# Optimization experiments

Measured on AMD Instinct MI355X. Metric: run time of the kernel, lower is better.

## Reference

```python
import jax, jax.numpy as jnp
import numpy as np

N, E, D_IN, H = 100000, 1000000, 128, 64


def setup_inputs() -> dict:
    key = jax.random.key(0)
    ks = jax.random.split(key, 8)
    return {
        "x": jax.random.normal(ks[0], (N, D_IN), dtype=jnp.float32),
        "edge_index": jax.random.randint(ks[1], (2, E), 0, N, dtype=jnp.int64),
        "W1": jax.random.normal(ks[2], (H, D_IN), dtype=jnp.float32) * (1.0 / np.sqrt(D_IN)),
        "b1": jax.random.normal(ks[3], (H,), dtype=jnp.float32) * 0.05,
        "Wmu": jax.random.normal(ks[4], (H, H), dtype=jnp.float32) * (1.0 / np.sqrt(H)),
        "bmu": jax.random.normal(ks[5], (H,), dtype=jnp.float32) * 0.05,
        "Wlv": jax.random.normal(ks[6], (H, H), dtype=jnp.float32) * (1.0 / np.sqrt(H)),
        "blv": jax.random.normal(ks[7], (H,), dtype=jnp.float32) * 0.05,
    }


def reference(x, edge_index, W1, b1, Wmu, bmu, Wlv, blv):
    n = x.shape[0]
    # GCNConv (PyG defaults): add self-loops, symmetric normalization
    loop = jnp.arange(n, dtype=edge_index.dtype)
    src = jnp.concatenate([edge_index[0], loop])  # [E+N]
    dst = jnp.concatenate([edge_index[1], loop])  # [E+N]
    deg = jax.ops.segment_sum(jnp.ones(src.shape[0], dtype=x.dtype), dst, num_segments=n)
    dinv = jnp.where(deg > 0, jax.lax.rsqrt(deg), 0.0)  # deg^{-1/2}
    norm = dinv[src] * dinv[dst]  # [E+N]
    h = x @ W1.T  # [N, H] linear transform before aggregation
    msg = h[src] * norm[:, None]  # gather + scale, [E+N, H]
    agg = jax.ops.segment_sum(msg, dst, num_segments=n) + b1  # scatter-add + bias
    h = jax.nn.relu(agg)
    return (h @ Wmu.T + bmu, h @ Wlv.T + blv)
```

## Files before the change

kernel.cpp:

```cpp
#include <hip/hip_runtime.h>

#define DIN 128
#define HDIM 64
#define SLAB 32
#define OVF_CAP 65536
#define EPT 4

__device__ __forceinline__ unsigned short f2bf(float f) {
    unsigned u = __float_as_uint(f);
    unsigned r = (u + 0x7fffu + ((u >> 16) & 1u)) >> 16;
    return (unsigned short)r;
}
__device__ __forceinline__ float lo16f(unsigned v) { return __uint_as_float(v << 16); }
__device__ __forceinline__ float hi16f(unsigned v) { return __uint_as_float(v & 0xffff0000u); }

__global__ __launch_bounds__(256) void k_scatter(const int* __restrict__ src,
                                                 const int* __restrict__ dst,
                                                 int* __restrict__ cursor,
                                                 int* __restrict__ slab,
                                                 int* __restrict__ ovf,
                                                 int* __restrict__ govf, int E) {
    int base = blockIdx.x * (256 * EPT) + threadIdx.x;
    int d[EPT], s[EPT], p[EPT];
    bool ok[EPT];
    #pragma unroll
    for (int q = 0; q < EPT; ++q) {
        int e = base + q * 256;
        ok[q] = e < E;
        d[q] = ok[q] ? dst[e] : 0;
        s[q] = ok[q] ? src[e] : 0;
    }
    #pragma unroll
    for (int q = 0; q < EPT; ++q)
        if (ok[q]) p[q] = atomicAdd(&cursor[d[q]], 1);
    #pragma unroll
    for (int q = 0; q < EPT; ++q) {
        if (ok[q]) {
            if (p[q] < SLAB) {
                slab[(size_t)d[q] * SLAB + p[q]] = s[q];
            } else {
                int o = atomicAdd(govf, 1);
                if (o < OVF_CAP) { ovf[2 * o] = d[q]; ovf[2 * o + 1] = s[q]; }
            }
        }
    }
}

__global__ __launch_bounds__(256) void k_h1(const float* __restrict__ x,
                                            const float* __restrict__ W1,
                                            const int* __restrict__ cursor,
                                            unsigned short* __restrict__ hs_bf, int n) {
    __shared__ float4 xs[64 * 32];
    __shared__ float4 ws[64 * 32];
    int t = threadIdx.x;
    int ty = t >> 4;
    int tx = t & 15;
    int nodeBase = blockIdx.x * 64;

    const float4* W14 = (const float4*)W1;
    #pragma unroll
    for (int i = 0; i < 8; ++i) {
        int f = t + i * 256;
        int r = f >> 5, c4 = f & 31;
        ws[r * 32 + (c4 ^ (r & 7))] = W14[f];
    }
    const float4* x4 = (const float4*)(x + (size_t)nodeBase * DIN);
    int limf4 = (n - nodeBase) * (DIN / 4);
    #pragma unroll
    for (int i = 0; i < 8; ++i) {
        int f = t + i * 256;
        int r = f >> 5, c4 = f & 31;
        float4 v = make_float4(0.f, 0.f, 0.f, 0.f);
        if (f < limf4) v = x4[f];
        xs[r * 32 + (c4 ^ (r & 7))] = v;
    }
    __syncthreads();

    float acc[4][4] = {};
    #pragma unroll 8
    for (int k4 = 0; k4 < 32; ++k4) {
        float4 xa[4], wb[4];
        #pragma unroll
        for (int i = 0; i < 4; ++i) {
            int r = ty + 16 * i;
            xa[i] = xs[r * 32 + (k4 ^ (r & 7))];
        }
        #pragma unroll
        for (int j = 0; j < 4; ++j) {
            int r = tx + 16 * j;
            wb[j] = ws[r * 32 + (k4 ^ (r & 7))];
        }
        #pragma unroll
        for (int i = 0; i < 4; ++i)
            #pragma unroll
            for (int j = 0; j < 4; ++j)
                acc[i][j] += xa[i].x * wb[j].x + xa[i].y * wb[j].y +
                             xa[i].z * wb[j].z + xa[i].w * wb[j].w;
    }

    #pragma unroll
    for (int i = 0; i < 4; ++i) {
        int node = nodeBase + ty + 16 * i;
        if (node < n) {
            float dn = rsqrtf((float)cursor[node] + 1.0f);
            #pragma unroll
            for (int j = 0; j < 4; ++j)
                hs_bf[(size_t)node * HDIM + tx + 16 * j] = f2bf(acc[i][j] * dn);
        }
    }
}

__global__ __launch_bounds__(256) void k_gather(const int* __restrict__ cursor,
                                                const int* __restrict__ slab,
                                                const unsigned short* __restrict__ hs_bf,
                                                float* __restrict__ h, int n) {
    int tid = threadIdx.x;
    int lane = tid & 63, wave = tid >> 6;
    int grp = lane >> 4;
    int w = lane & 15;
    const int NPW = 8;
    int base = blockIdx.x * (4 * NPW) + wave * NPW;
    for (int nn = 0; nn < NPW; ++nn) {
        int node = base + nn;
        if (node >= n) break;
        int c = cursor[node];
        int cs = (c < SLAB) ? c : SLAB;
        int sv = (lane < cs) ? slab[(size_t)node * SLAB + lane] : 0;
        uint2 v0 = *(const uint2*)(hs_bf + ((size_t)node << 6) + 4 * w);
        float sw = (grp == 0) ? 1.f : 0.f;
        float a0 = sw * lo16f(v0.x), a1 = sw * hi16f(v0.x);
        float a2 = sw * lo16f(v0.y), a3 = sw * hi16f(v0.y);
        int nfull = cs >> 2;
        for (int q = 0; q < nfull; ++q) {
            int s = __shfl(sv, 4 * q + grp);
            uint2 v = *(const uint2*)(hs_bf + ((size_t)s << 6) + 4 * w);
            a0 += lo16f(v.x); a1 += hi16f(v.x);
            a2 += lo16f(v.y); a3 += hi16f(v.y);
        }
        int r = cs & 3;
        if (r) {
            int e = 4 * nfull + grp;
            float wt = (grp < r) ? 1.f : 0.f;
            int s = __shfl(sv, (e < SLAB) ? e : 0);
            uint2 v = *(const uint2*)(hs_bf + ((size_t)s << 6) + 4 * w);
            a0 += wt * lo16f(v.x); a1 += wt * hi16f(v.x);
            a2 += wt * lo16f(v.y); a3 += wt * hi16f(v.y);
        }
        a0 += __shfl_xor(a0, 16); a0 += __shfl_xor(a0, 32);
        a1 += __shfl_xor(a1, 16); a1 += __shfl_xor(a1, 32);
        a2 += __shfl_xor(a2, 16); a2 += __shfl_xor(a2, 32);
        a3 += __shfl_xor(a3, 16); a3 += __shfl_xor(a3, 32);
        if (lane < 16)
            *(float4*)(h + ((size_t)node << 6) + 4 * w) = make_float4(a0, a1, a2, a3);
    }
}

__global__ __launch_bounds__(256) void k_overflow(const int* __restrict__ govf,
                                                  const int* __restrict__ ovf,
                                                  const unsigned short* __restrict__ hs_bf,
                                                  float* __restrict__ h) {
    int novf = govf[0];
    if (novf > OVF_CAP) novf = OVF_CAP;
    int wid = (blockIdx.x * 256 + threadIdx.x) >> 6;
    int lane = threadIdx.x & 63;
    int nw = (gridDim.x * 256) >> 6;
    for (int i = wid; i < novf; i += nw) {
        int d = ovf[2 * i], s = ovf[2 * i + 1];
        atomicAdd(&h[(size_t)d * HDIM + lane],
                  lo16f((unsigned)hs_bf[(size_t)s * HDIM + lane]));
    }
}

__global__ __launch_bounds__(256) void k_out(const float* __restrict__ h,
                                             const int* __restrict__ cursor,
                                             const float* __restrict__ b1,
                                             const float* __restrict__ Wmu,
                                             const float* __restrict__ bmu,
                                             const float* __restrict__ Wlv,
                                             const float* __restrict__ blv,
                                             float* __restrict__ out, int n) {
    __shared__ float4 xs[64 * 16];
    __shared__ float4 ws[128 * 16];
    int t = threadIdx.x;
    int ty = t >> 4;
    int tx = t & 15;
    int nodeBase = blockIdx.x * 64;

    const float4* Wm4 = (const float4*)Wmu;
    const float4* Wl4 = (const float4*)Wlv;
    #pragma unroll
    for (int i = 0; i < 4; ++i) {
        int f = t + i * 256;
        int r = f >> 4, c4 = f & 15;
        ws[r * 16 + (c4 ^ (r & 15))] = Wm4[f];
        int r2 = r + 64;
        ws[r2 * 16 + (c4 ^ (r2 & 15))] = Wl4[f];
    }
    const float4* h4 = (const float4*)(h + (size_t)nodeBase * HDIM);
    int limf4 = (n - nodeBase) * (HDIM / 4);
    #pragma unroll
    for (int i = 0; i < 4; ++i) {
        int f = t + i * 256;
        int r = f >> 4, c4 = f & 15;
        float4 v = make_float4(0.f, 0.f, 0.f, 0.f);
        if (f < limf4) {
            v = h4[f];
            float dn = rsqrtf((float)cursor[nodeBase + r] + 1.0f);
            float4 bb = ((const float4*)b1)[c4];
            v.x = fmaxf(fmaf(v.x, dn, bb.x), 0.f);
            v.y = fmaxf(fmaf(v.y, dn, bb.y), 0.f);
            v.z = fmaxf(fmaf(v.z, dn, bb.z), 0.f);
            v.w = fmaxf(fmaf(v.w, dn, bb.w), 0.f);
        }
        xs[r * 16 + (c4 ^ (r & 15))] = v;
    }
    float bias[8];
    #pragma unroll
    for (int j = 0; j < 8; ++j) {
        int o = tx + 16 * j;
        bias[j] = (o < 64) ? bmu[o] : blv[o - 64];
    }
    __syncthreads();

    float acc[4][8] = {};
    #pragma unroll 4
    for (int k4 = 0; k4 < 16; ++k4) {
        float4 xa[4], wb[8];
        #pragma unroll
        for (int i = 0; i < 4; ++i) {
            int r = ty + 16 * i;
            xa[i] = xs[r * 16 + (k4 ^ (r & 15))];
        }
        #pragma unroll
        for (int j = 0; j < 8; ++j) {
            int r = tx + 16 * j;
            wb[j] = ws[r * 16 + (k4 ^ (r & 15))];
        }
        #pragma unroll
        for (int i = 0; i < 4; ++i)
            #pragma unroll
            for (int j = 0; j < 8; ++j)
                acc[i][j] += xa[i].x * wb[j].x + xa[i].y * wb[j].y +
                             xa[i].z * wb[j].z + xa[i].w * wb[j].w;
    }

    #pragma unroll
    for (int i = 0; i < 4; ++i) {
        int node = nodeBase + ty + 16 * i;
        if (node < n) {
            #pragma unroll
            for (int j = 0; j < 8; ++j) {
                int o = tx + 16 * j;
                float val = acc[i][j] + bias[j];
                if (o < 64)
                    out[(size_t)node * HDIM + o] = val;
                else
                    out[(size_t)n * HDIM + (size_t)node * HDIM + (o - 64)] = val;
            }
        }
    }
}

extern "C" void kernel_launch(void* const* d_in, const int* in_sizes, int n_in,
                              void* d_out, int out_size, void* d_ws, size_t ws_size,
                              hipStream_t stream) {
    const float* x   = (const float*)d_in[0];
    const int*   ei  = (const int*)d_in[1];
    const float* W1  = (const float*)d_in[2];
    const float* b1  = (const float*)d_in[3];
    const float* Wmu = (const float*)d_in[4];
    const float* bmu = (const float*)d_in[5];
    const float* Wlv = (const float*)d_in[6];
    const float* blv = (const float*)d_in[7];
    float* out = (float*)d_out;

    const int N = in_sizes[0] / DIN;
    const int E = in_sizes[1] / 2;
    const int* src = ei;
    const int* dst = ei + E;

    auto align256 = [](size_t b) { return (b + 255) & ~(size_t)255; };
    char* ws = (char*)d_ws;
    size_t off = 0;
    int* cursor = (int*)(ws + off); off += align256((size_t)N * 4);
    int* govf   = (int*)(ws + off); off += 256;
    int* slab   = (int*)(ws + off); off += align256((size_t)N * SLAB * 4);
    int* ovf    = (int*)(ws + off); off += align256((size_t)OVF_CAP * 2 * 4);
    unsigned short* hs_bf = (unsigned short*)(ws + off);
    off += align256((size_t)N * HDIM * 2);
    float* h = (float*)(ws + off); off += align256((size_t)N * HDIM * 4);

    hipMemsetAsync(cursor, 0, align256((size_t)N * 4) + 256, stream);

    k_scatter<<<(E + 256 * EPT - 1) / (256 * EPT), 256, 0, stream>>>(src, dst, cursor,
                                                                     slab, ovf, govf, E);
    k_h1<<<(N + 63) / 64, 256, 0, stream>>>(x, W1, cursor, hs_bf, N);
    k_gather<<<(N + 31) / 32, 256, 0, stream>>>(cursor, slab, hs_bf, h, N);
    k_overflow<<<8, 256, 0, stream>>>(govf, ovf, hs_bf, h);
    k_out<<<(N + 63) / 64, 256, 0, stream>>>(h, cursor, b1, Wmu, bmu, Wlv, blv, out, N);
}
```

Measured before the change: 179.5 us.

## Merge edge scatter and x@W1 into one launch, add separate degree-scale pass

The edge-bucketing scatter and the x@W1 GEMM now run as one launch, with the block index choosing the role, so the atomic-heavy scatter and the compute-bound GEMM can overlap. The GEMM no longer depends on the degree counts, so the deg^-1/2 scaling moves into a new k_scale pass over hs_bf. That pass adds an extra read-modify-write of the bf16 buffer and a second bf16 rounding. The GEMM shared tile is halved into two K chunks, and the gather now uses 16-byte loads with 8 neighbours per wave step instead of 4.

```diff
diff --git a/kernel.cpp b/kernel.cpp
--- a/kernel.cpp
+++ b/kernel.cpp
@@ -14,100 +14,114 @@
 __device__ __forceinline__ float lo16f(unsigned v) { return __uint_as_float(v << 16); }
 __device__ __forceinline__ float hi16f(unsigned v) { return __uint_as_float(v & 0xffff0000u); }
 
-__global__ __launch_bounds__(256) void k_scatter(const int* __restrict__ src,
-                                                 const int* __restrict__ dst,
-                                                 int* __restrict__ cursor,
-                                                 int* __restrict__ slab,
-                                                 int* __restrict__ ovf,
-                                                 int* __restrict__ govf, int E) {
-    int base = blockIdx.x * (256 * EPT) + threadIdx.x;
-    int d[EPT], s[EPT], p[EPT];
-    bool ok[EPT];
-    #pragma unroll
-    for (int q = 0; q < EPT; ++q) {
-        int e = base + q * 256;
-        ok[q] = e < E;
-        d[q] = ok[q] ? dst[e] : 0;
-        s[q] = ok[q] ? src[e] : 0;
-    }
-    #pragma unroll
-    for (int q = 0; q < EPT; ++q)
-        if (ok[q]) p[q] = atomicAdd(&cursor[d[q]], 1);
-    #pragma unroll
-    for (int q = 0; q < EPT; ++q) {
-        if (ok[q]) {
-            if (p[q] < SLAB) {
-                slab[(size_t)d[q] * SLAB + p[q]] = s[q];
-            } else {
-                int o = atomicAdd(govf, 1);
-                if (o < OVF_CAP) { ovf[2 * o] = d[q]; ovf[2 * o + 1] = s[q]; }
+__global__ __launch_bounds__(256) void k_scatter_h1(
+        const int* __restrict__ src, const int* __restrict__ dst,
+        int* __restrict__ cursor, int* __restrict__ slab,
+        int* __restrict__ ovf, int* __restrict__ govf, int E,
+        const float* __restrict__ x, const float* __restrict__ W1,
+        unsigned short* __restrict__ hs_bf, int n, int scatBlocks) {
+    __shared__ float4 xs[64 * 16];
+    __shared__ float4 ws[64 * 16];
+    int t = threadIdx.x;
+
+    if ((int)blockIdx.x < scatBlocks) {
+        int base = blockIdx.x * (256 * EPT) + t;
+        int d[EPT], s[EPT], p[EPT];
+        bool ok[EPT];
+        #pragma unroll
+        for (int q = 0; q < EPT; ++q) {
+            int e = base + q * 256;
+            ok[q] = e < E;
+            d[q] = ok[q] ? dst[e] : 0;
+            s[q] = ok[q] ? src[e] : 0;
+        }
+        #pragma unroll
+        for (int q = 0; q < EPT; ++q)
+            if (ok[q]) p[q] = atomicAdd(&cursor[d[q]], 1);
+        #pragma unroll
+        for (int q = 0; q < EPT; ++q) {
+            if (ok[q]) {
+                if (p[q] < SLAB) {
+                    slab[(size_t)d[q] * SLAB + p[q]] = s[q];
+                } else {
+                    int o = atomicAdd(govf, 1);
+                    if (o < OVF_CAP) { ovf[2 * o] = d[q]; ovf[2 * o + 1] = s[q]; }
+                }
             }
         }
-    }
-}
-
-__global__ __launch_bounds__(256) void k_h1(const float* __restrict__ x,
-                                            const float* __restrict__ W1,
-                                            const int* __restrict__ cursor,
-                                            unsigned short* __restrict__ hs_bf, int n) {
-    __shared__ float4 xs[64 * 32];
-    __shared__ float4 ws[64 * 32];
-    int t = threadIdx.x;
+        return;
+    }
+
+    int bid = blockIdx.x - scatBlocks;
     int ty = t >> 4;
     int tx = t & 15;
-    int nodeBase = blockIdx.x * 64;
-
+    int nodeBase = bid * 64;
     const float4* W14 = (const float4*)W1;
-    #pragma unroll
-    for (int i = 0; i < 8; ++i) {
-        int f = t + i * 256;
-        int r = f >> 5, c4 = f & 31;
-        ws[r * 32 + (c4 ^ (r & 7))] = W14[f];
-    }
     const float4* x4 = (const float4*)(x + (size_t)nodeBase * DIN);
     int limf4 = (n - nodeBase) * (DIN / 4);
-    #pragma unroll
-    for (int i = 0; i < 8; ++i) {
-        int f = t + i * 256;
-        int r = f >> 5, c4 = f & 31;
-        float4 v = make_float4(0.f, 0.f, 0.f, 0.f);
-        if (f < limf4) v = x4[f];
-        xs[r * 32 + (c4 ^ (r & 7))] = v;
-    }
-    __syncthreads();
 
     float acc[4][4] = {};
-    #pragma unroll 8
-    for (int k4 = 0; k4 < 32; ++k4) {
-        float4 xa[4], wb[4];
+    #pragma unroll
+    for (int kc = 0; kc < 2; ++kc) {
         #pragma unroll
         for (int i = 0; i < 4; ++i) {
-            int r = ty + 16 * i;
-            xa[i] = xs[r * 32 + (k4 ^ (r & 7))];
-        }
-        #pragma unroll
-        for (int j = 0; j < 4; ++j) {
-            int r = tx + 16 * j;
-            wb[j] = ws[r * 32 + (k4 ^ (r & 7))];
-        }
-        #pragma unroll
-        for (int i = 0; i < 4; ++i)
-            #pragma unroll
-            for (int j = 0; j < 4; ++j)
-                acc[i][j] += xa[i].x * wb[j].x + xa[i].y * wb[j].y +
-                             xa[i].z * wb[j].z + xa[i].w * wb[j].w;
+            int e = t + i * 256;
+            int r = e >> 4, c4 = e & 15;
+            ws[r * 16 + (c4 ^ (r & 15))] = W14[r * 32 + kc * 16 + c4];
+            int f4 = r * 32 + kc * 16 + c4;
+            float4 v = make_float4(0.f, 0.f, 0.f, 0.f);
+            if (f4 < limf4) v = x4[f4];
+            xs[r * 16 + (c4 ^ (r & 15))] = v;
+        }
+        __syncthreads();
+        #pragma unroll 8
+        for (int k4 = 0; k4 < 16; ++k4) {
+            float4 xa[4], wb[4];
+            #pragma unroll
+            for (int i = 0; i < 4; ++i) {
+                int r = ty + 16 * i;
+                xa[i] = xs[r * 16 + (k4 ^ (r & 15))];
+            }
+            #pragma unroll
+            for (int j = 0; j < 4; ++j) {
+                int r = tx + 16 * j;
+                wb[j] = ws[r * 16 + (k4 ^ (r & 15))];
+            }
+            #pragma unroll
+            for (int i = 0; i < 4; ++i)
+                #pragma unroll
+                for (int j = 0; j < 4; ++j)
+                    acc[i][j] += xa[i].x * wb[j].x + xa[i].y * wb[j].y +
+                                 xa[i].z * wb[j].z + xa[i].w * wb[j].w;
+        }
+        __syncthreads();
     }
 
     #pragma unroll
     for (int i = 0; i < 4; ++i) {
         int node = nodeBase + ty + 16 * i;
         if (node < n) {
-            float dn = rsqrtf((float)cursor[node] + 1.0f);
             #pragma unroll
             for (int j = 0; j < 4; ++j)
-                hs_bf[(size_t)node * HDIM + tx + 16 * j] = f2bf(acc[i][j] * dn);
-        }
-    }
+                hs_bf[(size_t)node * HDIM + tx + 16 * j] = f2bf(acc[i][j]);
+        }
+    }
+}
+
+__global__ __launch_bounds__(256) void k_scale(const int* __restrict__ cursor,
+                                               unsigned short* __restrict__ hs_bf, int n) {
+    int t = blockIdx.x * 256 + threadIdx.x;
+    int node = t >> 3;
+    if (node >= n) return;
+    float dn = rsqrtf((float)cursor[node] + 1.0f);
+    unsigned* p = (unsigned*)(hs_bf + ((size_t)node << 6) + 8 * (t & 7));
+    uint4 v = *(uint4*)p;
+    uint4 o;
+    o.x = (unsigned)f2bf(lo16f(v.x) * dn) | ((unsigned)f2bf(hi16f(v.x) * dn) << 16);
+    o.y = (unsigned)f2bf(lo16f(v.y) * dn) | ((unsigned)f2bf(hi16f(v.y) * dn) << 16);
+    o.z = (unsigned)f2bf(lo16f(v.z) * dn) | ((unsigned)f2bf(hi16f(v.z) * dn) << 16);
+    o.w = (unsigned)f2bf(lo16f(v.w) * dn) | ((unsigned)f2bf(hi16f(v.w) * dn) << 16);
+    *(uint4*)p = o;
 }
 
 __global__ __launch_bounds__(256) void k_gather(const int* __restrict__ cursor,
@@ -116,8 +130,8 @@
                                                 float* __restrict__ h, int n) {
     int tid = threadIdx.x;
     int lane = tid & 63, wave = tid >> 6;
-    int grp = lane >> 4;
-    int w = lane & 15;
+    int grp = lane >> 3;
+    int w8 = lane & 7;
     const int NPW = 8;
     int base = blockIdx.x * (4 * NPW) + wave * NPW;
     for (int nn = 0; nn < NPW; ++nn) {
@@ -126,32 +140,40 @@
         int c = cursor[node];
         int cs = (c < SLAB) ? c : SLAB;
         int sv = (lane < cs) ? slab[(size_t)node * SLAB + lane] : 0;
-        uint2 v0 = *(const uint2*)(hs_bf + ((size_t)node << 6) + 4 * w);
+        uint4 v0 = *(const uint4*)(hs_bf + ((size_t)node << 6) + 8 * w8);
         float sw = (grp == 0) ? 1.f : 0.f;
         float a0 = sw * lo16f(v0.x), a1 = sw * hi16f(v0.x);
         float a2 = sw * lo16f(v0.y), a3 = sw * hi16f(v0.y);
-        int nfull = cs >> 2;
+        float a4 = sw * lo16f(v0.z), a5 = sw * hi16f(v0.z);
+        float a6 = sw * lo16f(v0.w), a7 = sw * hi16f(v0.w);
+        int nfull = cs >> 3;
         for (int q = 0; q < nfull; ++q) {
-            int s = __shfl(sv, 4 * q + grp);
-            uint2 v = *(const uint2*)(hs_bf + ((size_t)s << 6) + 4 * w);
+            int s = __shfl(sv, 8 * q + grp);
+            uint4 v = *(const uint4*)(hs_bf + ((size_t)s << 6) + 8 * w8);
             a0 += lo16f(v.x); a1 += hi16f(v.x);
             a2 += lo16f(v.y); a3 += hi16f(v.y);
-        }
-        int r = cs & 3;
+            a4 += lo16f(v.z); a5 += hi16f(v.z);
+            a6 += lo16f(v.w); a7 += hi16f(v.w);
+        }
+        int r = cs & 7;
         if (r) {
-            int e = 4 * nfull + grp;
+            int e = 8 * nfull + grp;
             float wt = (grp < r) ? 1.f : 0.f;
             int s = __shfl(sv, (e < SLAB) ? e : 0);
-            uint2 v = *(const uint2*)(hs_bf + ((size_t)s << 6) + 4 * w);
+            uint4 v = *(const uint4*)(hs_bf + ((size_t)s << 6) + 8 * w8);
             a0 += wt * lo16f(v.x); a1 += wt * hi16f(v.x);
             a2 += wt * lo16f(v.y); a3 += wt * hi16f(v.y);
-        }
-        a0 += __shfl_xor(a0, 16); a0 += __shfl_xor(a0, 32);
-        a1 += __shfl_xor(a1, 16); a1 += __shfl_xor(a1, 32);
-        a2 += __shfl_xor(a2, 16); a2 += __shfl_xor(a2, 32);
-        a3 += __shfl_xor(a3, 16); a3 += __shfl_xor(a3, 32);
-        if (lane < 16)
-            *(float4*)(h + ((size_t)node << 6) + 4 * w) = make_float4(a0, a1, a2, a3);
+            a4 += wt * lo16f(v.z); a5 += wt * hi16f(v.z);
+            a6 += wt * lo16f(v.w); a7 += wt * hi16f(v.w);
+        }
+        #define RED(A) A += __shfl_xor(A, 8); A += __shfl_xor(A, 16); A += __shfl_xor(A, 32);
+        RED(a0) RED(a1) RED(a2) RED(a3) RED(a4) RED(a5) RED(a6) RED(a7)
+        #undef RED
+        if (lane < 8) {
+            float* hp = h + ((size_t)node << 6) + 8 * w8;
+            *(float4*)hp = make_float4(a0, a1, a2, a3);
+            *(float4*)(hp + 4) = make_float4(a4, a5, a6, a7);
+        }
     }
 }
 
@@ -292,9 +314,11 @@
 
     hipMemsetAsync(cursor, 0, align256((size_t)N * 4) + 256, stream);
 
-    k_scatter<<<(E + 256 * EPT - 1) / (256 * EPT), 256, 0, stream>>>(src, dst, cursor,
-                                                                     slab, ovf, govf, E);
-    k_h1<<<(N + 63) / 64, 256, 0, stream>>>(x, W1, cursor, hs_bf, N);
+    int scatBlocks = (E + 256 * EPT - 1) / (256 * EPT);
+    int h1Blocks = (N + 63) / 64;
+    k_scatter_h1<<<scatBlocks + h1Blocks, 256, 0, stream>>>(
+        src, dst, cursor, slab, ovf, govf, E, x, W1, hs_bf, N, scatBlocks);
+    k_scale<<<(N * 8 + 255) / 256, 256, 0, stream>>>(cursor, hs_bf, N);
     k_gather<<<(N + 31) / 32, 256, 0, stream>>>(cursor, slab, hs_bf, h, N);
     k_overflow<<<8, 256, 0, stream>>>(govf, ovf, hs_bf, h);
     k_out<<<(N + 63) / 64, 256, 0, stream>>>(h, cursor, b1, Wmu, bmu, Wlv, blv, out, N);
```

After: 167.5 us. 1.07x faster.
